# Performance work log

Measured on AMD Instinct MI355X. Metric: run time of the kernel, lower is better.

The kernel has to match this reference:

```python
import jax, jax.numpy as jnp
import numpy as np

C = 768
HEADS = 12

def setup_inputs() -> dict:
    key = jax.random.key(0)
    k1, k2, k3 = jax.random.split(key, 3)
    x = jax.random.normal(k1, (8, C, 32, 32), dtype=jnp.float32)
    # 1x1 convs are channel-wise linear maps; store as [out_c, in_c]
    w_qkv = jax.random.normal(k2, (3 * C, C), dtype=jnp.float32) * (C ** -0.5)
    w_proj = jax.random.normal(k3, (C, C), dtype=jnp.float32) * (C ** -0.5)
    return {"x": x, "w_qkv": w_qkv, "w_proj": w_proj}

def reference(x, w_qkv, w_proj):
    b, c, h, w = x.shape
    heads = HEADS
    dh = c // heads
    n = h * w
    scale = dh ** -0.5
    # 1x1 conv QKV: [b, 3c, h, w] -> [b, 3, heads, dh, n]
    qkv = jnp.einsum('oc,bchw->bohw', w_qkv, x).reshape(b, 3, heads, dh, n)
    q, k, v = qkv[:, 0], qkv[:, 1], qkv[:, 2]  # each [b, heads, dh, n]
    attn = jnp.einsum('bhdn,bhdm->bhnm', q, k) * scale  # [b, heads, n, n]
    attn = jax.nn.softmax(attn, axis=-1)
    out = jnp.einsum('bhnm,bhdm->bhdn', attn, v)  # [b, heads, dh, n]
    out = out.reshape(b, c, h, w)
    return jnp.einsum('oc,bchw->bohw', w_proj, out)
```

## Files before the change

### kernel.cpp

```cpp
#include <hip/hip_runtime.h>

typedef unsigned short u16;
typedef unsigned int u32;
typedef float v4f __attribute__((ext_vector_type(4)));
typedef __bf16 bf16x8 __attribute__((ext_vector_type(8)));

#define BATCH 8
#define CDIM 768
#define NHEAD 12
#define DH 64
#define NSEQ 1024
#define SCL 0.18033688011112042f

__device__ __forceinline__ u16 f2bf(float f) {
  u32 u = __builtin_bit_cast(u32, f);
  u += 0x7fffu + ((u >> 16) & 1u);
  return (u16)(u >> 16);
}

__device__ __forceinline__ u16 b16(float f) {
  return (u16)((__builtin_bit_cast(u32, f) + 0x8000u) >> 16);
}

__device__ __forceinline__ u32 pkbf(float hi, float lo) {
  u32 a = __builtin_bit_cast(u32, hi) + 0x8000u;
  u32 b = __builtin_bit_cast(u32, lo) + 0x8000u;
  return __builtin_amdgcn_perm(a, b, 0x07060302u);
}

__device__ __forceinline__ v4f mfma16(bf16x8 a, bf16x8 b, v4f c) {
  return __builtin_amdgcn_mfma_f32_16x16x32_bf16(a, b, c, 0, 0, 0);
}

__device__ __forceinline__ void gload16(const u16* g, u16* l) {
  __builtin_amdgcn_global_load_lds(
      (const __attribute__((address_space(1))) void*)g,
      (__attribute__((address_space(3))) void*)l, 16, 0, 0);
}

#define BARQ asm volatile("s_barrier" ::: "memory")
#define LGKM0 asm volatile("s_waitcnt lgkmcnt(0)" ::: "memory")
#define VMC0 asm volatile("s_waitcnt vmcnt(0)" ::: "memory")
#define FEN asm volatile("" ::: "memory")

__global__ __launch_bounds__(256) void k_prep(const float* __restrict__ x,
                                              const float* __restrict__ wq,
                                              const float* __restrict__ wp,
                                              u16* __restrict__ xT,
                                              u16* __restrict__ wqb,
                                              u16* __restrict__ wpb) {
  __shared__ u16 Ts[64][72];
  int bid = blockIdx.x;
  int t = threadIdx.x;
  if (bid < 2304) {
    bool isQ = bid < 1728;
    const float* s = isQ ? wq : wp;
    u16* d = isQ ? wqb : wpb;
    int i = (isQ ? bid : bid - 1728) * 256 + t;
    float4 v = ((const float4*)s)[i];
    u32 lo = (u32)f2bf(v.x) | ((u32)f2bf(v.y) << 16);
    u32 hi = (u32)f2bf(v.z) | ((u32)f2bf(v.w) << 16);
    ((uint2*)d)[i] = uint2{lo, hi};
    return;
  }
  int id = bid - 2304;
  int p0 = (id & 15) * 64; id >>= 4;
  int c0 = (id % 12) * 64; int b = id / 12;
  int cr = t >> 4;
  int p4 = (t & 15) * 4;
  const float* src = x + ((size_t)b * CDIM + c0) * NSEQ + p0;
#pragma unroll
  for (int i = 0; i < 4; ++i) {
    int c = cr + i * 16;
    float4 v = *(const float4*)&src[(size_t)c * NSEQ + p4];
    Ts[p4 + 0][c] = f2bf(v.x);
    Ts[p4 + 1][c] = f2bf(v.y);
    Ts[p4 + 2][c] = f2bf(v.z);
    Ts[p4 + 3][c] = f2bf(v.w);
  }
  __syncthreads();
  int p = t >> 2;
  int cq = t & 3;
  u16* dst = xT + ((size_t)b * NSEQ + p0 + p) * CDIM + c0;
#pragma unroll
  for (int j = 0; j < 2; ++j) {
    int ch = cq + j * 4;
    *(int4*)&dst[ch * 8] = *(const int4*)&Ts[p][ch * 8];
  }
}

#define NKT 24

__global__ __launch_bounds__(512, 2) void k_gemm_qkv(const u16* __restrict__ Wb,
                                                     const u16* __restrict__ xT,
                                                     u16* __restrict__ qkT,
                                                     u16* __restrict__ vbuf) {
  __shared__ u16 sm[3 * 17408];
  int bid = blockIdx.x;
  int swz = (bid & 7) * 32 + (bid >> 3);
  int oIdx = swz % 8, pIdx = swz / 8;
  int oT = oIdx * 288;
  int pG = pIdx * 256;

  int t = threadIdx.x, lane = t & 63, wid = t >> 6;
  int ln = lane & 15, quad = lane >> 4;
  int wm = wid >> 2, wn = wid & 3;

  int lrow = lane >> 2;
  int scg = ((lane & 3) ^ ((lane >> 3) & 3)) * 8;
  bool roleA = wid < 6;
  int w6 = wid - 6;
  const u16* Asrc = Wb + (size_t)(oT + wid * 48 + lrow) * CDIM + scg;
  const u16* Bsrc = xT + (size_t)(pG + (w6 < 0 ? 0 : w6) * 128 + lrow) * CDIM + scg;
  int ldA = wid * 1536;
  int ldB = 9216 + (w6 < 0 ? 0 : w6) * 4096;

#define STAGEQ(bi, kt) do {                                                \
    u16* bb_ = sm + (bi) * 17408;                                          \
    if (roleA) {                                                           \
      const u16* gp_ = Asrc + (kt) * 32;                                   \
      gload16(gp_, bb_ + ldA);                                             \
      gload16(gp_ + (size_t)16 * CDIM, bb_ + ldA + 512);                   \
      gload16(gp_ + (size_t)32 * CDIM, bb_ + ldA + 1024);                  \
    } else {                                                               \
      const u16* gp_ = Bsrc + (kt) * 32;                                   \
      _Pragma("unroll") for (int i_ = 0; i_ < 8; ++i_)                     \
        gload16(gp_ + (size_t)i_ * 16 * CDIM, bb_ + ldB + i_ * 512);       \
    }                                                                      \
  } while (0)

#define DRAINQ do {                                                        \
    if (roleA) asm volatile("s_waitcnt vmcnt(3)" ::: "memory");            \
    else asm volatile("s_waitcnt vmcnt(8)" ::: "memory");                  \
  } while (0)

  int slot = (quad ^ ((ln >> 1) & 3)) * 8;
  int rAr = (wm * 144 + ln) * 32;
  int rBr = 9216 + (wn * 64 + ln) * 32;

  v4f acc[9][4] = {};

  STAGEQ(0, 0);
  FEN;
  STAGEQ(1, 1);
  DRAINQ;
  BARQ;

  for (int j = 0; j < NKT; ++j) {
    const u16* sb = sm + (j % 3) * 17408;
    int bi2 = (j + 2) % 3;

    if (j < NKT - 2) STAGEQ(bi2, j + 2);
    bf16x8 af[5], bfr[4];
#pragma unroll
    for (int m = 0; m < 5; ++m)
      af[m] = *(const bf16x8*)&sb[rAr + m * 512 + slot];
#pragma unroll
    for (int n = 0; n < 4; ++n)
      bfr[n] = *(const bf16x8*)&sb[rBr + n * 512 + slot];
    BARQ;
    LGKM0;
    __builtin_amdgcn_sched_barrier(0);
    __builtin_amdgcn_s_setprio(1);
#pragma unroll
    for (int m = 0; m < 5; ++m)
#pragma unroll
      for (int n = 0; n < 4; ++n)
        acc[m][n] = mfma16(af[m], bfr[n], acc[m][n]);
    __builtin_amdgcn_s_setprio(0);
    BARQ;

    bf16x8 ag[4];
#pragma unroll
    for (int m = 0; m < 4; ++m)
      ag[m] = *(const bf16x8*)&sb[rAr + (m + 5) * 512 + slot];
    if (j < NKT - 2) DRAINQ;
    else if (j == NKT - 2) VMC0;
    BARQ;
    LGKM0;
    __builtin_amdgcn_sched_barrier(0);
    __builtin_amdgcn_s_setprio(1);
#pragma unroll
    for (int m = 0; m < 4; ++m)
#pragma unroll
      for (int n = 0; n < 4; ++n)
        acc[m + 5][n] = mfma16(ag[m], bfr[n], acc[m + 5][n]);
    __builtin_amdgcn_s_setprio(0);
    BARQ;
  }

#pragma unroll
  for (int m = 0; m < 9; ++m) {
#pragma unroll
    for (int n = 0; n < 4; ++n) {
      int ro = oT + wm * 144 + m * 16 + quad * 4;
      int cp = pG + wn * 64 + n * 16 + ln;
      int b = cp >> 10, p = cp & 1023;
      if (ro < 2 * CDIM) {
        u32 lo = (u32)f2bf(acc[m][n][0]) | ((u32)f2bf(acc[m][n][1]) << 16);
        u32 hi = (u32)f2bf(acc[m][n][2]) | ((u32)f2bf(acc[m][n][3]) << 16);
        *(uint2*)&qkT[((size_t)b * NSEQ + p) * 1536 + ro] = uint2{lo, hi};
      } else {
#pragma unroll
        for (int r = 0; r < 4; ++r)
          vbuf[((size_t)b * CDIM + (ro - 2 * CDIM + r)) * NSEQ + p] =
              f2bf(acc[m][n][r]);
      }
    }
  }
#undef STAGEQ
#undef DRAINQ
}

__device__ __forceinline__ void gemm_core(const u16* __restrict__ Ag,
                                          const u16* __restrict__ Bg,
                                          u16* sm, v4f (&acc)[8][4]) {
  int t = threadIdx.x, lane = t & 63, wid = t >> 6;
  int ln = lane & 15, quad = lane >> 4;
  int wm = wid >> 1, wn = wid & 1;

  int srow = wid * 16 + (lane >> 2);
  int scg = ((lane & 3) ^ ((lane >> 3) & 3)) * 8;
  const u16* As0 = Ag + (size_t)srow * CDIM + scg;
  const u16* Bs0 = Bg + (size_t)srow * CDIM + scg;
  int ldw = wid * 512;

  int cA = (quad ^ ((ln >> 1) & 3)) * 8;
  int rA = (wm * 128 + ln) * 32;
  int rB = 8192 + (wn * 64 + ln) * 32;

  {
    u16* sb0 = sm;
    gload16(As0, sb0 + ldw);
    gload16(As0 + (size_t)64 * CDIM, sb0 + 2048 + ldw);
    gload16(As0 + (size_t)128 * CDIM, sb0 + 4096 + ldw);
    gload16(As0 + (size_t)192 * CDIM, sb0 + 6144 + ldw);
    gload16(Bs0, sb0 + 8192 + ldw);
    gload16(Bs0 + (size_t)64 * CDIM, sb0 + 10240 + ldw);
  }
  FEN;
  {
    u16* sb1 = sm + 12288;
    gload16(As0 + 32, sb1 + ldw);
    gload16(As0 + (size_t)64 * CDIM + 32, sb1 + 2048 + ldw);
    gload16(As0 + (size_t)128 * CDIM + 32, sb1 + 4096 + ldw);
    gload16(As0 + (size_t)192 * CDIM + 32, sb1 + 6144 + ldw);
    gload16(Bs0 + 32, sb1 + 8192 + ldw);
    gload16(Bs0 + (size_t)64 * CDIM + 32, sb1 + 10240 + ldw);
  }
  asm volatile("s_waitcnt vmcnt(6)" ::: "memory");
  BARQ;

  for (int kb = 0; kb < 8; ++kb) {
#pragma unroll
    for (int u = 0; u < 3; ++u) {
      int kt = kb * 3 + u;
      const u16* sb = sm + u * 12288;
      u16* nb = sm + ((u + 2) % 3) * 12288;
      int ko = (kt + 2) * 32;

      bf16x8 af[4], bfr[4];
#pragma unroll
      for (int m = 0; m < 4; ++m)
        af[m] = *(const bf16x8*)&sb[rA + m * 512 + cA];
#pragma unroll
      for (int n = 0; n < 4; ++n)
        bfr[n] = *(const bf16x8*)&sb[rB + n * 512 + cA];
      if (kt < NKT - 2) {
        gload16(As0 + ko, nb + ldw);
        gload16(As0 + (size_t)64 * CDIM + ko, nb + 2048 + ldw);
        gload16(Bs0 + ko, nb + 8192 + ldw);
      }
      BARQ;
      LGKM0;
      __builtin_amdgcn_sched_barrier(0);
      __builtin_amdgcn_s_setprio(1);
#pragma unroll
      for (int m = 0; m < 4; ++m)
#pragma unroll
        for (int n = 0; n < 4; ++n)
          acc[m][n] = mfma16(af[m], bfr[n], acc[m][n]);
      __builtin_amdgcn_s_setprio(0);
      BARQ;

#pragma unroll
      for (int m = 0; m < 4; ++m)
        af[m] = *(const bf16x8*)&sb[rA + (m + 4) * 512 + cA];
      if (kt < NKT - 2) {
        gload16(As0 + (size_t)128 * CDIM + ko, nb + 4096 + ldw);
        gload16(As0 + (size_t)192 * CDIM + ko, nb + 6144 + ldw);
        gload16(Bs0 + (size_t)64 * CDIM + ko, nb + 10240 + ldw);
        asm volatile("s_waitcnt vmcnt(6)" ::: "memory");
      } else if (kt == NKT - 2) {
        VMC0;
      }
      BARQ;
      LGKM0;
      __builtin_amdgcn_sched_barrier(0);
      __builtin_amdgcn_s_setprio(1);
#pragma unroll
      for (int m = 0; m < 4; ++m)
#pragma unroll
        for (int n = 0; n < 4; ++n)
          acc[m + 4][n] = mfma16(af[m], bfr[n], acc[m + 4][n]);
      __builtin_amdgcn_s_setprio(0);
      BARQ;
    }
  }
}

__global__ __launch_bounds__(256) void k_attn(const u16* __restrict__ qkT,
                                              const u16* __restrict__ vbuf,
                                              u16* __restrict__ attnT) {
  int id = blockIdx.x;
  int b = id & 7;
  int j = id >> 3;
  int h = j % 12;
  int nt0 = (j / 12) * 128;

  int t = threadIdx.x, lane = t & 63, wid = t >> 6;
  int ln = lane & 15, quad = lane >> 4;
  int nbase = nt0 + wid * 32;

  __shared__ u16 Ks[2][64 * 64];
  __shared__ u16 Vs[2][64 * 64];
  __shared__ u16 Pa[4][32 * 64];
  u16* myP = Pa[wid];

  const u16* qbase = qkT + ((size_t)b * NSEQ + nbase) * 1536 + h * DH;
  bf16x8 aq[2][2];
#pragma unroll
  for (int mt = 0; mt < 2; ++mt)
#pragma unroll
    for (int ks = 0; ks < 2; ++ks)
      aq[mt][ks] = *(const bf16x8*)&qbase[(size_t)(mt * 16 + ln) * 1536 + ks * 32 + quad * 8];

  bf16x8 ones;
#pragma unroll
  for (int i = 0; i < 8; ++i) ones[i] = __builtin_bit_cast(__bf16, (u16)0x3F80);

  v4f oacc[2][4] = {};
  v4f lacc[2] = {};

  int sr8 = lane >> 3;
  int sch = ((lane & 7) ^ sr8) * 8;
  const u16* kg0 = qkT + ((size_t)b * NSEQ + wid * 16 + sr8) * 1536 + CDIM + h * DH + sch;
  const u16* vg0 = vbuf + ((size_t)b * CDIM + h * DH + wid * 16 + sr8) * NSEQ + sch;
  int sK = (wid * 16) * 64;

  int sw0 = (quad ^ (ln & 7)) * 8;
  int sw1 = ((4 + quad) ^ (ln & 7)) * 8;
  int e7 = ln & 7;

  gload16(kg0, &Ks[0][sK]);
  gload16(kg0 + (size_t)8 * 1536, &Ks[0][sK + 512]);
  gload16(vg0, &Vs[0][sK]);
  gload16(vg0 + 8 * NSEQ, &Vs[0][sK + 512]);
  __syncthreads();

  for (int s = 0; s < 16; ++s) {
    int cur = s & 1, nxt = cur ^ 1;
    if (s < 15) {
      size_t ko = (size_t)(s + 1) * 64 * 1536;
      int vo = (s + 1) * 64;
      gload16(kg0 + ko, &Ks[nxt][sK]);
      gload16(kg0 + ko + (size_t)8 * 1536, &Ks[nxt][sK + 512]);
      gload16(vg0 + vo, &Vs[nxt][sK]);
      gload16(vg0 + vo + 8 * NSEQ, &Vs[nxt][sK + 512]);
    }

#pragma unroll
    for (int ct = 0; ct < 4; ++ct) {
      bf16x8 kf0 = *(const bf16x8*)&Ks[cur][(ct * 16 + ln) * 64 + sw0];
      bf16x8 kf1 = *(const bf16x8*)&Ks[cur][(ct * 16 + ln) * 64 + sw1];
#pragma unroll
      for (int mt = 0; mt < 2; ++mt) {
        v4f sc = {};
        __builtin_amdgcn_s_setprio(1);
        sc = mfma16(kf0, aq[mt][0], sc);
        sc = mfma16(kf1, aq[mt][1], sc);
        __builtin_amdgcn_s_setprio(0);
        float p0 = __builtin_amdgcn_exp2f(sc[0] * SCL);
        float p1 = __builtin_amdgcn_exp2f(sc[1] * SCL);
        float p2 = __builtin_amdgcn_exp2f(sc[2] * SCL);
        float p3 = __builtin_amdgcn_exp2f(sc[3] * SCL);
        int woff = (mt * 16 + ln) * 64 +
                   (((2 * ct + (quad >> 1)) ^ e7) * 8 + (quad & 1) * 4);
        *(uint2*)&myP[woff] = uint2{pkbf(p1, p0), pkbf(p3, p2)};
      }
    }

    bf16x8 ap[2][2];
#pragma unroll
    for (int mt = 0; mt < 2; ++mt)
#pragma unroll
      for (int ks = 0; ks < 2; ++ks)
        ap[mt][ks] = *(const bf16x8*)&myP[(mt * 16 + ln) * 64 +
                                          ((ks * 4 + quad) ^ e7) * 8];
    __builtin_amdgcn_s_setprio(1);
#pragma unroll
    for (int mt = 0; mt < 2; ++mt) {
      lacc[mt] = mfma16(ap[mt][0], ones, lacc[mt]);
      lacc[mt] = mfma16(ap[mt][1], ones, lacc[mt]);
    }
    __builtin_amdgcn_s_setprio(0);
#pragma unroll
    for (int nt = 0; nt < 4; ++nt) {
      bf16x8 vf0 = *(const bf16x8*)&Vs[cur][(nt * 16 + ln) * 64 + sw0];
      bf16x8 vf1 = *(const bf16x8*)&Vs[cur][(nt * 16 + ln) * 64 + sw1];
      __builtin_amdgcn_s_setprio(1);
#pragma unroll
      for (int mt = 0; mt < 2; ++mt) {
        oacc[mt][nt] = mfma16(ap[mt][0], vf0, oacc[mt][nt]);
        oacc[mt][nt] = mfma16(ap[mt][1], vf1, oacc[mt][nt]);
      }
      __builtin_amdgcn_s_setprio(0);
    }
    __syncthreads();
  }

#pragma unroll
  for (int mt = 0; mt < 2; ++mt) {
#pragma unroll
    for (int r = 0; r < 4; ++r) {
      float inv = 1.0f / lacc[mt][r];
      int n = nbase + mt * 16 + quad * 4 + r;
      u16* dst = attnT + ((size_t)b * NSEQ + n) * CDIM + h * DH;
#pragma unroll
      for (int nt = 0; nt < 4; ++nt)
        dst[nt * 16 + ln] = b16(oacc[mt][nt][r] * inv);
    }
  }
}

__global__ __launch_bounds__(256, 2) void k_gemm_proj(const u16* __restrict__ Wb,
                                                      const u16* __restrict__ aT,
                                                      float* __restrict__ out) {
  __shared__ u16 sm[3 * 12288];
  int bid = blockIdx.x;
  int swz = (bid & 7) * 24 + (bid >> 3);
  int oIdx = swz % 3, pIdx = swz / 3;
  int oT = oIdx * 256;
  int pG = pIdx * 128;

  v4f acc[8][4] = {};
  gemm_core(Wb + (size_t)oT * CDIM, aT + (size_t)pG * CDIM, sm, acc);

  int t = threadIdx.x, lane = t & 63, wid = t >> 6;
  int ln = lane & 15, quad = lane >> 4;
  int wm = wid >> 1, wn = wid & 1;
#pragma unroll
  for (int m = 0; m < 8; ++m) {
#pragma unroll
    for (int n = 0; n < 4; ++n) {
      int ro = oT + wm * 128 + m * 16 + quad * 4;
      int cp = pG + wn * 64 + n * 16 + ln;
      int b = cp >> 10, p = cp & 1023;
#pragma unroll
      for (int r = 0; r < 4; ++r)
        out[((size_t)b * CDIM + ro + r) * NSEQ + p] = acc[m][n][r];
    }
  }
}

extern "C" void kernel_launch(void* const* d_in, const int* in_sizes, int n_in,
                              void* d_out, int out_size, void* d_ws, size_t ws_size,
                              hipStream_t stream) {
  const float* x = (const float*)d_in[0];
  const float* w_qkv = (const float*)d_in[1];
  const float* w_proj = (const float*)d_in[2];
  float* out = (float*)d_out;

  char* ws = (char*)d_ws;
  u16* wqkv_bf = (u16*)(ws);
  u16* wproj_bf = (u16*)(ws + 3538944);
  u16* xT = (u16*)(ws + 4718592);
  u16* vbuf = (u16*)(ws + 17301504);
  u16* qkT = (u16*)d_out;
  u16* attnT = xT;

  k_prep<<<dim3(3840), dim3(256), 0, stream>>>(x, w_qkv, w_proj, xT, wqkv_bf, wproj_bf);
  k_gemm_qkv<<<dim3(256), dim3(512), 0, stream>>>(wqkv_bf, xT, qkT, vbuf);
  k_attn<<<dim3(768), dim3(256), 0, stream>>>(qkT, vbuf, attnT);
  k_gemm_proj<<<dim3(192), dim3(256), 0, stream>>>(wproj_bf, attnT, out);
}
```

Before: 177.8 us.

## Retile projection GEMM to 192x128 so grid covers all CUs

```diff
diff --git a/kernel.cpp b/kernel.cpp
--- a/kernel.cpp
+++ b/kernel.cpp
@@ -212,103 +212,6 @@
 #undef DRAINQ
 }
 
-__device__ __forceinline__ void gemm_core(const u16* __restrict__ Ag,
-                                          const u16* __restrict__ Bg,
-                                          u16* sm, v4f (&acc)[8][4]) {
-  int t = threadIdx.x, lane = t & 63, wid = t >> 6;
-  int ln = lane & 15, quad = lane >> 4;
-  int wm = wid >> 1, wn = wid & 1;
-
-  int srow = wid * 16 + (lane >> 2);
-  int scg = ((lane & 3) ^ ((lane >> 3) & 3)) * 8;
-  const u16* As0 = Ag + (size_t)srow * CDIM + scg;
-  const u16* Bs0 = Bg + (size_t)srow * CDIM + scg;
-  int ldw = wid * 512;
-
-  int cA = (quad ^ ((ln >> 1) & 3)) * 8;
-  int rA = (wm * 128 + ln) * 32;
-  int rB = 8192 + (wn * 64 + ln) * 32;
-
-  {
-    u16* sb0 = sm;
-    gload16(As0, sb0 + ldw);
-    gload16(As0 + (size_t)64 * CDIM, sb0 + 2048 + ldw);
-    gload16(As0 + (size_t)128 * CDIM, sb0 + 4096 + ldw);
-    gload16(As0 + (size_t)192 * CDIM, sb0 + 6144 + ldw);
-    gload16(Bs0, sb0 + 8192 + ldw);
-    gload16(Bs0 + (size_t)64 * CDIM, sb0 + 10240 + ldw);
-  }
-  FEN;
-  {
-    u16* sb1 = sm + 12288;
-    gload16(As0 + 32, sb1 + ldw);
-    gload16(As0 + (size_t)64 * CDIM + 32, sb1 + 2048 + ldw);
-    gload16(As0 + (size_t)128 * CDIM + 32, sb1 + 4096 + ldw);
-    gload16(As0 + (size_t)192 * CDIM + 32, sb1 + 6144 + ldw);
-    gload16(Bs0 + 32, sb1 + 8192 + ldw);
-    gload16(Bs0 + (size_t)64 * CDIM + 32, sb1 + 10240 + ldw);
-  }
-  asm volatile("s_waitcnt vmcnt(6)" ::: "memory");
-  BARQ;
-
-  for (int kb = 0; kb < 8; ++kb) {
-#pragma unroll
-    for (int u = 0; u < 3; ++u) {
-      int kt = kb * 3 + u;
-      const u16* sb = sm + u * 12288;
-      u16* nb = sm + ((u + 2) % 3) * 12288;
-      int ko = (kt + 2) * 32;
-
-      bf16x8 af[4], bfr[4];
-#pragma unroll
-      for (int m = 0; m < 4; ++m)
-        af[m] = *(const bf16x8*)&sb[rA + m * 512 + cA];
-#pragma unroll
-      for (int n = 0; n < 4; ++n)
-        bfr[n] = *(const bf16x8*)&sb[rB + n * 512 + cA];
-      if (kt < NKT - 2) {
-        gload16(As0 + ko, nb + ldw);
-        gload16(As0 + (size_t)64 * CDIM + ko, nb + 2048 + ldw);
-        gload16(Bs0 + ko, nb + 8192 + ldw);
-      }
-      BARQ;
-      LGKM0;
-      __builtin_amdgcn_sched_barrier(0);
-      __builtin_amdgcn_s_setprio(1);
-#pragma unroll
-      for (int m = 0; m < 4; ++m)
-#pragma unroll
-        for (int n = 0; n < 4; ++n)
-          acc[m][n] = mfma16(af[m], bfr[n], acc[m][n]);
-      __builtin_amdgcn_s_setprio(0);
-      BARQ;
-
-#pragma unroll
-      for (int m = 0; m < 4; ++m)
-        af[m] = *(const bf16x8*)&sb[rA + (m + 4) * 512 + cA];
-      if (kt < NKT - 2) {
-        gload16(As0 + (size_t)128 * CDIM + ko, nb + 4096 + ldw);
-        gload16(As0 + (size_t)192 * CDIM + ko, nb + 6144 + ldw);
-        gload16(Bs0 + (size_t)64 * CDIM + ko, nb + 10240 + ldw);
-        asm volatile("s_waitcnt vmcnt(6)" ::: "memory");
-      } else if (kt == NKT - 2) {
-        VMC0;
-      }
-      BARQ;
-      LGKM0;
-      __builtin_amdgcn_sched_barrier(0);
-      __builtin_amdgcn_s_setprio(1);
-#pragma unroll
-      for (int m = 0; m < 4; ++m)
-#pragma unroll
-        for (int n = 0; n < 4; ++n)
-          acc[m + 4][n] = mfma16(af[m], bfr[n], acc[m + 4][n]);
-      __builtin_amdgcn_s_setprio(0);
-      BARQ;
-    }
-  }
-}
-
 __global__ __launch_bounds__(256) void k_attn(const u16* __restrict__ qkT,
                                               const u16* __restrict__ vbuf,
                                               u16* __restrict__ attnT) {
@@ -436,24 +339,103 @@
 __global__ __launch_bounds__(256, 2) void k_gemm_proj(const u16* __restrict__ Wb,
                                                       const u16* __restrict__ aT,
                                                       float* __restrict__ out) {
-  __shared__ u16 sm[3 * 12288];
+  __shared__ u16 sm[3 * 10240];
   int bid = blockIdx.x;
-  int swz = (bid & 7) * 24 + (bid >> 3);
-  int oIdx = swz % 3, pIdx = swz / 3;
-  int oT = oIdx * 256;
+  int swz = (bid & 7) * 32 + (bid >> 3);
+  int oIdx = swz % 4, pIdx = swz / 4;
+  int oT = oIdx * 192;
   int pG = pIdx * 128;
-
-  v4f acc[8][4] = {};
-  gemm_core(Wb + (size_t)oT * CDIM, aT + (size_t)pG * CDIM, sm, acc);
 
   int t = threadIdx.x, lane = t & 63, wid = t >> 6;
   int ln = lane & 15, quad = lane >> 4;
   int wm = wid >> 1, wn = wid & 1;
-#pragma unroll
-  for (int m = 0; m < 8; ++m) {
+
+  int lrow = lane >> 2;
+  int scg = ((lane & 3) ^ ((lane >> 3) & 3)) * 8;
+  bool roleA = wid < 3;
+  const u16* Asrc = Wb + (size_t)(oT + wid * 64 + lrow) * CDIM + scg;
+  const u16* Bsrc = aT + (size_t)(pG + lrow) * CDIM + scg;
+  int ldA = wid * 2048;
+  int ldB = 6144;
+
+#define STAGEP(bi, kt) do {                                                \
+    u16* bb_ = sm + (bi) * 10240;                                          \
+    if (roleA) {                                                           \
+      const u16* gp_ = Asrc + (kt) * 32;                                   \
+      _Pragma("unroll") for (int i_ = 0; i_ < 4; ++i_)                     \
+        gload16(gp_ + (size_t)i_ * 16 * CDIM, bb_ + ldA + i_ * 512);       \
+    } else {                                                               \
+      const u16* gp_ = Bsrc + (kt) * 32;                                   \
+      _Pragma("unroll") for (int i_ = 0; i_ < 8; ++i_)                     \
+        gload16(gp_ + (size_t)i_ * 16 * CDIM, bb_ + ldB + i_ * 512);       \
+    }                                                                      \
+  } while (0)
+
+#define DRAINP do {                                                        \
+    if (roleA) asm volatile("s_waitcnt vmcnt(4)" ::: "memory");            \
+    else asm volatile("s_waitcnt vmcnt(8)" ::: "memory");                  \
+  } while (0)
+
+  int slot = (quad ^ ((ln >> 1) & 3)) * 8;
+  int rAr = (wm * 96 + ln) * 32;
+  int rBr = 6144 + (wn * 64 + ln) * 32;
+
+  v4f acc[6][4] = {};
+
+  STAGEP(0, 0);
+  FEN;
+  STAGEP(1, 1);
+  DRAINP;
+  BARQ;
+
+  for (int j = 0; j < NKT; ++j) {
+    const u16* sb = sm + (j % 3) * 10240;
+    int bi2 = (j + 2) % 3;
+
+    if (j < NKT - 2) STAGEP(bi2, j + 2);
+    bf16x8 af[3], bfr[4];
+#pragma unroll
+    for (int m = 0; m < 3; ++m)
+      af[m] = *(const bf16x8*)&sb[rAr + m * 512 + slot];
+#pragma unroll
+    for (int n = 0; n < 4; ++n)
+      bfr[n] = *(const bf16x8*)&sb[rBr + n * 512 + slot];
+    BARQ;
+    LGKM0;
+    __builtin_amdgcn_sched_barrier(0);
+    __builtin_amdgcn_s_setprio(1);
+#pragma unroll
+    for (int m = 0; m < 3; ++m)
+#pragma unroll
+      for (int n = 0; n < 4; ++n)
+        acc[m][n] = mfma16(af[m], bfr[n], acc[m][n]);
+    __builtin_amdgcn_s_setprio(0);
+    BARQ;
+
+    bf16x8 ag[3];
+#pragma unroll
+    for (int m = 0; m < 3; ++m)
+      ag[m] = *(const bf16x8*)&sb[rAr + (m + 3) * 512 + slot];
+    if (j < NKT - 2) DRAINP;
+    else if (j == NKT - 2) VMC0;
+    BARQ;
+    LGKM0;
+    __builtin_amdgcn_sched_barrier(0);
+    __builtin_amdgcn_s_setprio(1);
+#pragma unroll
+    for (int m = 0; m < 3; ++m)
+#pragma unroll
+      for (int n = 0; n < 4; ++n)
+        acc[m + 3][n] = mfma16(ag[m], bfr[n], acc[m + 3][n]);
+    __builtin_amdgcn_s_setprio(0);
+    BARQ;
+  }
+
+#pragma unroll
+  for (int m = 0; m < 6; ++m) {
 #pragma unroll
     for (int n = 0; n < 4; ++n) {
-      int ro = oT + wm * 128 + m * 16 + quad * 4;
+      int ro = oT + wm * 96 + m * 16 + quad * 4;
       int cp = pG + wn * 64 + n * 16 + ln;
       int b = cp >> 10, p = cp & 1023;
 #pragma unroll
@@ -461,6 +443,8 @@
         out[((size_t)b * CDIM + ro + r) * NSEQ + p] = acc[m][n][r];
     }
   }
+#undef STAGEP
+#undef DRAINP
 }
 
 extern "C" void kernel_launch(void* const* d_in, const int* in_sizes, int n_in,
@@ -482,5 +466,5 @@
   k_prep<<<dim3(3840), dim3(256), 0, stream>>>(x, w_qkv, w_proj, xT, wqkv_bf, wproj_bf);
   k_gemm_qkv<<<dim3(256), dim3(512), 0, stream>>>(wqkv_bf, xT, qkT, vbuf);
   k_attn<<<dim3(768), dim3(256), 0, stream>>>(qkT, vbuf, attnT);
-  k_gemm_proj<<<dim3(192), dim3(256), 0, stream>>>(wproj_bf, attnT, out);
-}
+  k_gemm_proj<<<dim3(256), dim3(256), 0, stream>>>(wproj_bf, attnT, out);
+}
```

Result: no change. 176.6 us (-0.7%).
